# Kernel optimization log

Hardware: AMD Instinct MI355X
Metric: run time of the kernel (lower is better)

The kernel has to match this reference:

```python
import jax, jax.numpy as jnp
import numpy as np

IN_Q, OUT_Q = 32, 32
GRID_H, GRID_W = 64, 64
FREQ_H, FREQ_W = GRID_H, GRID_W // 2 + 1
BATCH = 32
INIT_SCALE = 0.02


def setup_inputs() -> dict:
    key = jax.random.key(0)
    keys = jax.random.split(key, 9)
    inp = {"x": jax.random.normal(keys[0], (BATCH, 4 * IN_Q, GRID_H, GRID_W), dtype=jnp.float32)}
    names = ["kr_w", "kr_x", "kr_y", "kr_z", "ki_w", "ki_x", "ki_y", "ki_z"]
    for i, n in enumerate(names):
        inp[n] = jax.random.normal(keys[i + 1], (IN_Q, OUT_Q, FREQ_H, FREQ_W), dtype=jnp.float32) * INIT_SCALE
    return inp


def reference(x, kr_w, kr_x, kr_y, kr_z, ki_w, ki_x, ki_y, ki_z):
    q = IN_Q
    # Split quaternion components and FFT each: [B, q, H, Wf] complex
    xs = jnp.stack([x[:, :q], x[:, q:2 * q], x[:, 2 * q:3 * q], x[:, 3 * q:]])  # [4,B,q,H,W]
    Xs = jnp.fft.rfft2(xs, s=(GRID_H, GRID_W), axes=(-2, -1))  # [4,B,q,H,Wf]
    # Complex kernels, stacked: [4, in_q, out_q, H, Wf]
    Ws = jnp.stack([kr_w + 1j * ki_w, kr_x + 1j * ki_x, kr_y + 1j * ki_y, kr_z + 1j * ki_z])
    # All 16 pairwise contractions in one einsum: C[p,q] = W_p contracted with X_q
    C = jnp.einsum('piohw,qbihw->pqbohw', Ws, Xs)  # [4,4,B,out,H,Wf]
    # Hamilton product combination
    Pw = C[0, 0] - C[1, 1] - C[2, 2] - C[3, 3]
    Px = C[0, 1] + C[1, 0] + C[2, 3] - C[3, 2]
    Py = C[0, 2] - C[1, 3] + C[2, 0] + C[3, 1]
    Pz = C[0, 3] + C[1, 2] - C[2, 1] + C[3, 0]
    P = jnp.stack([Pw, Px, Py, Pz])  # [4,B,out,H,Wf]
    o = jnp.fft.irfft2(P, s=(GRID_H, GRID_W), axes=(-2, -1))  # [4,B,out,H,W]
    # cat along channel dim: [B, 4*out, H, W]
    return jnp.concatenate([o[0], o[1], o[2], o[3]], axis=1)
```

## Files before the change

kernel.cpp:

```cpp
#include <hip/hip_runtime.h>

#define FH 64
#define FW 64
#define NWF 33
#define NBIN (FH*NWF)
#define NIMG 4096
#define PI2 6.283185307179586f

typedef unsigned short u16;
typedef unsigned int u32;
typedef __attribute__((ext_vector_type(8))) short bf16x8;
typedef __attribute__((ext_vector_type(8))) _Float16 f16x8;
typedef __attribute__((ext_vector_type(4))) unsigned short u16x4;
typedef __attribute__((ext_vector_type(4))) float f32x4;
typedef __attribute__((ext_vector_type(4))) int   i32x4;

__device__ __forceinline__ u16 f2bf(float f) {
    unsigned u = __float_as_uint(f);
    unsigned r = (u + 0x7FFFu + ((u >> 16) & 1u)) >> 16;
    return (u16)r;
}
__device__ __forceinline__ u16 f2h(float f) {
    _Float16 h = (_Float16)f;
    return __builtin_bit_cast(u16, h);
}
__device__ __forceinline__ float2 upk(u32 v) {
    return make_float2(__uint_as_float(v << 16), __uint_as_float(v & 0xFFFF0000u));
}
__device__ __forceinline__ u32 pk(float2 v) {
    return (u32)f2bf(v.x) | ((u32)f2bf(v.y) << 16);
}
__device__ __forceinline__ f16x8 negh(f16x8 v) {
    i32x4 t = __builtin_bit_cast(i32x4, v);
    t ^= (int)0x80008000;
    return __builtin_bit_cast(f16x8, t);
}

__global__ __launch_bounds__(512, 4) void fwd_prep_kernel(
    const float* __restrict__ x, u32* __restrict__ Xs,
    const float* __restrict__ s0, const float* __restrict__ s1,
    const float* __restrict__ s2, const float* __restrict__ s3,
    const float* __restrict__ s4, const float* __restrict__ s5,
    const float* __restrict__ s6, const float* __restrict__ s7,
    u16* __restrict__ WT)
{
    __shared__ __align__(16) u16 sm[36864];
    const int tid = threadIdx.x;

    if (blockIdx.x < 1024) {
        const int lane = tid & 63;
        const int wid  = tid >> 6;
        const int slot = wid >> 1;
        const int half = wid & 1;
        const int a16  = lane & 15;
        const int q    = lane >> 4;

        const int img = blockIdx.x * 4 + slot;
        const int qc = img >> 10;
        const int b  = (img >> 5) & 31;
        const int ci = img & 31;
        const float* __restrict__ src = x + ((size_t)b*128 + (size_t)qc*32 + ci) * (FH*FW);

        u16* mats0 = sm;
        u16* mats1 = sm + 64*72;
        u16* ST    = sm + 9216 + slot*6912;

        for (int t = tid; t < 4096; t += 512) {
            int a = t >> 6, bb = t & 63;
            float sn, cs;
            __sincosf(PI2 * (float)((a*bb) & 63) * (1.f/64.f), &sn, &cs);
            mats0[a*72 + bb] = f2h(cs);
            mats1[a*72 + bb] = f2h(sn);
        }

        f16x8 xf[2][2];
        #pragma unroll
        for (int mtl = 0; mtl < 2; ++mtl)
            #pragma unroll
            for (int ks = 0; ks < 2; ++ks) {
                const float* rp = src + (16*(2*half + mtl) + a16)*64 + ks*32 + q*8;
                float4 v0 = *(const float4*)rp;
                float4 v1 = *(const float4*)(rp + 4);
                xf[mtl][ks] = (f16x8){ (_Float16)v0.x, (_Float16)v0.y, (_Float16)v0.z, (_Float16)v0.w,
                                       (_Float16)v1.x, (_Float16)v1.y, (_Float16)v1.z, (_Float16)v1.w };
            }
        __syncthreads();

        #pragma unroll
        for (int mtl = 0; mtl < 2; ++mtl) {
            const int mt = 2*half + mtl;
            f32x4 are[3], aim[3];
            #pragma unroll
            for (int nt = 0; nt < 3; ++nt) { are[nt] = (f32x4){0,0,0,0}; aim[nt] = (f32x4){0,0,0,0}; }
            #pragma unroll
            for (int nt = 0; nt < 3; ++nt)
                #pragma unroll
                for (int ks = 0; ks < 2; ++ks) {
                    const int rb = (16*nt + a16)*72 + ks*32 + q*8;
                    f16x8 cf = *(const f16x8*)&mats0[rb];
                    f16x8 sf = *(const f16x8*)&mats1[rb];
                    are[nt] = __builtin_amdgcn_mfma_f32_16x16x32_f16(xf[mtl][ks], cf, are[nt], 0, 0, 0);
                    aim[nt] = __builtin_amdgcn_mfma_f32_16x16x32_f16(xf[mtl][ks], negh(sf), aim[nt], 0, 0, 0);
                }
            const int hb = 16*mt + 4*q;
            #pragma unroll
            for (int nt = 0; nt < 3; ++nt) {
                u16x4 re4 = { f2h(are[nt][0]), f2h(are[nt][1]), f2h(are[nt][2]), f2h(are[nt][3]) };
                u16x4 im4 = { f2h(aim[nt][0]), f2h(aim[nt][1]), f2h(aim[nt][2]), f2h(aim[nt][3]) };
                *(u16x4*)&ST[(16*nt + a16)*72 + hb]      = re4;
                *(u16x4*)&ST[(48 + 16*nt + a16)*72 + hb] = im4;
            }
        }
        __syncthreads();

        f16x8 bfr[2][3][2];
        #pragma unroll
        for (int ri = 0; ri < 2; ++ri)
            #pragma unroll
            for (int nt = 0; nt < 3; ++nt)
                #pragma unroll
                for (int ks = 0; ks < 2; ++ks)
                    bfr[ri][nt][ks] = *(const f16x8*)&ST[(ri*48 + 16*nt + a16)*72 + ks*32 + q*8];

        u32* __restrict__ dst = Xs + (size_t)img * NBIN;
        #pragma unroll
        for (int mtl = 0; mtl < 2; ++mtl) {
            const int mt = 2*half + mtl;
            f16x8 cfa[2], sfa[2], nsf[2];
            #pragma unroll
            for (int ks = 0; ks < 2; ++ks) {
                const int rb = (16*mt + a16)*72 + ks*32 + q*8;
                cfa[ks] = *(const f16x8*)&mats0[rb];
                sfa[ks] = *(const f16x8*)&mats1[rb];
                nsf[ks] = negh(sfa[ks]);
            }
            #pragma unroll
            for (int nt = 0; nt < 3; ++nt) {
                f32x4 xre = (f32x4){0,0,0,0}, xim = (f32x4){0,0,0,0};
                #pragma unroll
                for (int ks = 0; ks < 2; ++ks) {
                    xre = __builtin_amdgcn_mfma_f32_16x16x32_f16(cfa[ks], bfr[0][nt][ks], xre, 0, 0, 0);
                    xre = __builtin_amdgcn_mfma_f32_16x16x32_f16(sfa[ks], bfr[1][nt][ks], xre, 0, 0, 0);
                    xim = __builtin_amdgcn_mfma_f32_16x16x32_f16(cfa[ks], bfr[1][nt][ks], xim, 0, 0, 0);
                    xim = __builtin_amdgcn_mfma_f32_16x16x32_f16(nsf[ks], bfr[0][nt][ks], xim, 0, 0, 0);
                }
                const int k = 16*nt + a16;
                if (k < 33) {
                    #pragma unroll
                    for (int r = 0; r < 4; ++r)
                        dst[(16*mt + 4*q + r)*33 + k] = pk(make_float2(xre[r], xim[r]));
                }
            }
        }
    } else {
        const int pb = blockIdx.x - 1024;
        const int bt = pb % 66;
        const int ay = pb / 66;
        const int a  = ay >> 2;
        const int o0 = (ay & 3) * 8;
        const float* __restrict__ src =
            (a==0)?s0:(a==1)?s1:(a==2)?s2:(a==3)?s3:(a==4)?s4:(a==5)?s5:(a==6)?s6:s7;
        const int bin0 = bt * 32;
        u16* lds2 = sm;

        #pragma unroll
        for (int it = 0; it < 4; ++it) {
            int e = tid + it*512;
            int f4 = e & 7, rt = e >> 3;
            int i = rt & 31, oo = rt >> 5;
            int io = i*32 + o0 + oo;
            float4 v = ((const float4*)src)[(size_t)io*(NBIN/4) + bt*8 + f4];
            int chL = oo*32 + i;
            int bb = f4*4;
            lds2[(bb+0)*264 + chL] = f2bf(v.x);
            lds2[(bb+1)*264 + chL] = f2bf(v.y);
            lds2[(bb+2)*264 + chL] = f2bf(v.z);
            lds2[(bb+3)*264 + chL] = f2bf(v.w);
        }
        __syncthreads();
        const int p = a & 3, ri = a >> 2;
        #pragma unroll
        for (int it = 0; it < 2; ++it) {
            int e = tid + it*512;
            int binL = e >> 5, c8 = e & 31;
            bf16x8 v = *(const bf16x8*)&lds2[binL*264 + c8*8];
            size_t d = ((size_t)(bin0 + binL)*8 + p*2 + ri)*1024 + o0*32 + c8*8;
            *(bf16x8*)(WT + d) = v;
        }
    }
}

__global__ __launch_bounds__(256) void xpose_x_kernel(const u32* __restrict__ Xs,
                                                      u32* __restrict__ XT)
{
    const int g    = blockIdx.x;
    const int bin0 = blockIdx.y * 32;
    __shared__ u32 tile[32][33];
    const int tid = threadIdx.x;
    #pragma unroll
    for (int it = 0; it < 4; ++it) {
        int e = tid + it*256;
        int imgL = e >> 5, binL = e & 31;
        tile[imgL][binL] = Xs[(size_t)(g*32 + imgL) * NBIN + bin0 + binL];
    }
    __syncthreads();
    const int q = g >> 5, b = g & 31;
    #pragma unroll
    for (int it = 0; it < 2; ++it) {
        int e = tid + it*256;
        int binL = e >> 4, pr = e & 15;
        u32 v0 = tile[pr*2][binL], v1 = tile[pr*2 + 1][binL];
        u32 re = (v0 & 0xFFFFu) | (v1 << 16);
        u32 im = (v0 >> 16) | (v1 & 0xFFFF0000u);
        size_t base = ((size_t)(bin0 + binL)*8 + q*2) * 512 + b*16 + pr;
        XT[base]       = re;
        XT[base + 512] = im;
    }
}

__global__ __launch_bounds__(256) void contract_kernel(
    const u16* __restrict__ XT, const u16* __restrict__ WT,
    u32* __restrict__ P)
{
    const int bid  = blockIdx.x;
    const int bin  = (bid & 7) * (NBIN/8) + (bid >> 3);
    const int wid  = threadIdx.x >> 6;
    const int lane = threadIdx.x & 63;
    const int bh = wid >> 1, oh = wid & 1;
    const int row = lane & 15, kg = lane >> 4;

    const u16* __restrict__ xb = XT + (size_t)bin * 8192;
    const u16* __restrict__ wb = WT + (size_t)bin * 8192;

    bf16x8 ax[4][2];
    #pragma unroll
    for (int q = 0; q < 4; ++q)
        #pragma unroll
        for (int ri = 0; ri < 2; ++ri)
            ax[q][ri] = *(const bf16x8*)(xb + ((q*2 + ri)*32 + bh*16 + row)*32 + kg*8);

    bf16x8 wpos[4][2], wneg[4][2];
    #pragma unroll
    for (int p = 0; p < 4; ++p)
        #pragma unroll
        for (int ri = 0; ri < 2; ++ri) {
            bf16x8 w = *(const bf16x8*)(wb + ((p*2 + ri)*32 + oh*16 + row)*32 + kg*8);
            wpos[p][ri] = w;
            i32x4 t = __builtin_bit_cast(i32x4, w);
            t ^= (int)0x80008000;
            wneg[p][ri] = __builtin_bit_cast(bf16x8, t);
        }

    f32x4 acc[4][2];
    #pragma unroll
    for (int c = 0; c < 4; ++c)
        #pragma unroll
        for (int ri = 0; ri < 2; ++ri)
            acc[c][ri] = (f32x4){0.f, 0.f, 0.f, 0.f};

    constexpr int PI_[4][4] = {{0,1,2,3},{1,0,3,2},{2,3,0,1},{3,2,1,0}};
    constexpr int SG_[4][4] = {{1,-1,-1,-1},{1,1,-1,1},{1,1,1,-1},{1,-1,1,1}};
    #pragma unroll
    for (int c = 0; c < 4; ++c)
        #pragma unroll
        for (int q = 0; q < 4; ++q) {
            const int  p   = PI_[c][q];
            const bool pos = SG_[c][q] > 0;
            bf16x8 wr_s = pos ? wpos[p][0] : wneg[p][0];
            bf16x8 wi_s = pos ? wpos[p][1] : wneg[p][1];
            bf16x8 wi_m = pos ? wneg[p][1] : wpos[p][1];
            acc[c][0] = __builtin_amdgcn_mfma_f32_16x16x32_bf16(ax[q][0], wr_s, acc[c][0], 0, 0, 0);
            acc[c][0] = __builtin_amdgcn_mfma_f32_16x16x32_bf16(ax[q][1], wi_m, acc[c][0], 0, 0, 0);
            acc[c][1] = __builtin_amdgcn_mfma_f32_16x16x32_bf16(ax[q][1], wr_s, acc[c][1], 0, 0, 0);
            acc[c][1] = __builtin_amdgcn_mfma_f32_16x16x32_bf16(ax[q][0], wi_s, acc[c][1], 0, 0, 0);
        }

    u32* __restrict__ dst = P + (size_t)bin * 4096;
    #pragma unroll
    for (int c = 0; c < 4; ++c)
        #pragma unroll
        for (int r = 0; r < 4; ++r) {
            int b_ = bh*16 + kg*4 + r;
            int o  = oh*16 + row;
            dst[c*1024 + b_*32 + o] = pk(make_float2(acc[c][0][r], acc[c][1][r]));
        }
}

__global__ __launch_bounds__(512, 4) void fft_inv_kernel(const u32* __restrict__ P,
                                                         float* __restrict__ out)
{
    __shared__ __align__(16) u16 mats[2][64*72];
    __shared__ __align__(16) u16 wbuf[4][7168];

    const int tid  = threadIdx.x;
    const int lane = tid & 63;
    const int wid  = tid >> 6;
    const int slot = wid >> 1;
    const int half = wid & 1;
    const int ltid = (half << 6) | lane;
    const int a16  = lane & 15;
    const int q    = lane >> 4;

    const int bid = blockIdx.x;
    const int g   = (bid & 7) * 128 + (bid >> 3);
    const int img = g * 4 + slot;
    const int c  = img >> 10;
    const int b  = (img >> 5) & 31;
    const int oc = img & 31;

    for (int t = tid; t < 4096; t += 512) {
        int a = t >> 6, bb = t & 63;
        float sn, cs;
        __sincosf(PI2 * (float)((a*bb) & 63) * (1.f/64.f), &sn, &cs);
        mats[0][a*72 + bb] = f2h(cs);
        mats[1][a*72 + bb] = f2h(sn);
    }

    {
        u16* ETre = wbuf[slot];
        u16* ETim = wbuf[slot] + 48*72;
        for (int j = 33*72 + ltid; j < 48*72; j += 128) {
            ETre[j] = 0;
            ETim[j] = 0;
        }
    }
    for (int e = tid; e < NBIN*4; e += 512) {
        int bin = e >> 2, sl = e & 3;
        u32 v = P[(size_t)bin * 4096 + g*4 + sl];
        float2 f = upk(v);
        int hf = bin / 33, k = bin - hf*33;
        u16* ETre = wbuf[sl];
        u16* ETim = wbuf[sl] + 48*72;
        ETre[k*72 + hf] = f2h(f.x);
        ETim[k*72 + hf] = f2h(f.y);
    }
    __syncthreads();

    u16* ETre = wbuf[slot];
    u16* ETim = wbuf[slot] + 48*72;
    f16x8 ere[2][2], eim[2][2];
    #pragma unroll
    for (int mtl = 0; mtl < 2; ++mtl) {
        const int mt = 2*half + mtl;
        if (mt < 3) {
            #pragma unroll
            for (int ks = 0; ks < 2; ++ks) {
                ere[mtl][ks] = *(const f16x8*)&ETre[(16*mt + a16)*72 + ks*32 + q*8];
                eim[mtl][ks] = *(const f16x8*)&ETim[(16*mt + a16)*72 + ks*32 + q*8];
            }
        }
    }
    __syncthreads();

    u16* Tre = wbuf[slot];
    u16* Tim = wbuf[slot] + 64*56;
    #pragma unroll
    for (int mtl = 0; mtl < 2; ++mtl) {
        const int mt = 2*half + mtl;
        if (mt < 3) {
            #pragma unroll
            for (int nt = 0; nt < 4; ++nt) {
                f32x4 tre = (f32x4){0,0,0,0}, tim = (f32x4){0,0,0,0};
                #pragma unroll
                for (int ks = 0; ks < 2; ++ks) {
                    const int rb = (16*nt + a16)*72 + ks*32 + q*8;
                    f16x8 cf = *(const f16x8*)&mats[0][rb];
                    f16x8 sf = *(const f16x8*)&mats[1][rb];
                    tre = __builtin_amdgcn_mfma_f32_16x16x32_f16(ere[mtl][ks], cf, tre, 0, 0, 0);
                    tre = __builtin_amdgcn_mfma_f32_16x16x32_f16(eim[mtl][ks], negh(sf), tre, 0, 0, 0);
                    tim = __builtin_amdgcn_mfma_f32_16x16x32_f16(ere[mtl][ks], sf, tim, 0, 0, 0);
                    tim = __builtin_amdgcn_mfma_f32_16x16x32_f16(eim[mtl][ks], cf, tim, 0, 0, 0);
                }
                const int m0 = 16*mt + 4*q;
                u16x4 r4, i4;
                #pragma unroll
                for (int r = 0; r < 4; ++r) {
                    int m = m0 + r;
                    float s = (m == 0 || m == 32) ? (1.f/4096.f) : (2.f/4096.f);
                    r4[r] = (m < 33) ? f2h(tre[r] * s) : (u16)0;
                    i4[r] = (m < 33) ? f2h(tim[r] * s) : (u16)0;
                }
                *(u16x4*)&Tre[(16*nt + a16)*56 + m0] = r4;
                *(u16x4*)&Tim[(16*nt + a16)*56 + m0] = i4;
            }
        }
    }
    __syncthreads();

    float* __restrict__ dst = out + ((size_t)b*128 + (size_t)c*32 + oc) * (FH*FW);
    #pragma unroll
    for (int mtl = 0; mtl < 2; ++mtl) {
        const int mt = 2*half + mtl;
        f16x8 tfr[2], tfi[2];
        #pragma unroll
        for (int ks = 0; ks < 2; ++ks) {
            const int mbase = ks*32 + q*8;
            if (mbase < 48) {
                tfr[ks] = *(const f16x8*)&Tre[(16*mt + a16)*56 + mbase];
                tfi[ks] = *(const f16x8*)&Tim[(16*mt + a16)*56 + mbase];
            } else {
                tfr[ks] = (f16x8){0,0,0,0,0,0,0,0};
                tfi[ks] = (f16x8){0,0,0,0,0,0,0,0};
            }
        }
        #pragma unroll
        for (int nt = 0; nt < 4; ++nt) {
            f32x4 acc = (f32x4){0,0,0,0};
            #pragma unroll
            for (int ks = 0; ks < 2; ++ks) {
                const int rb = (16*nt + a16)*72 + ks*32 + q*8;
                f16x8 cf = *(const f16x8*)&mats[0][rb];
                f16x8 sf = *(const f16x8*)&mats[1][rb];
                acc = __builtin_amdgcn_mfma_f32_16x16x32_f16(tfr[ks], cf, acc, 0, 0, 0);
                acc = __builtin_amdgcn_mfma_f32_16x16x32_f16(tfi[ks], negh(sf), acc, 0, 0, 0);
            }
            #pragma unroll
            for (int r = 0; r < 4; ++r)
                dst[(16*mt + 4*q + r)*64 + 16*nt + a16] = acc[r];
        }
    }
}

extern "C" void kernel_launch(void* const* d_in, const int* in_sizes, int n_in,
                              void* d_out, int out_size, void* d_ws, size_t ws_size,
                              hipStream_t stream)
{
    const float* x   = (const float*)d_in[0];
    const float* krw = (const float*)d_in[1];
    const float* krx = (const float*)d_in[2];
    const float* kry = (const float*)d_in[3];
    const float* krz = (const float*)d_in[4];
    const float* kiw = (const float*)d_in[5];
    const float* kix = (const float*)d_in[6];
    const float* kiy = (const float*)d_in[7];
    const float* kiz = (const float*)d_in[8];

    const size_t R = (size_t)NBIN * 8192 * sizeof(u16);
    u16* XT = (u16*)d_ws;
    u16* WT = (u16*)((char*)d_ws + R);
    u32* Xs = (u32*)((char*)d_ws + 2*R);
    u32* P  = Xs;
    float* out = (float*)d_out;

    fwd_prep_kernel<<<dim3(1024 + 2112), 512, 0, stream>>>(x, Xs,
                                                           krw, krx, kry, krz,
                                                           kiw, kix, kiy, kiz, WT);
    xpose_x_kernel<<<dim3(128, NBIN/32), 256, 0, stream>>>(Xs, (u32*)XT);
    contract_kernel<<<dim3(NBIN), 256, 0, stream>>>(XT, WT, P);
    fft_inv_kernel<<<dim3(NIMG/4), 512, 0, stream>>>(P, out);
}
```

Measured before the change: 102.8 us.

## Process two image batches per FFT block and interleave FFT with weight-prep blocks

Each forward-FFT block now handles eight images in two rounds instead of four. It builds the twiddle table once for both rounds and issues the global loads for the second batch while the first batch's row pass is still running. Block indices are regrouped so that every 41 blocks hold 8 FFT blocks and 33 weight-transpose blocks, mixing compute-heavy and memory-heavy work across CUs. This adds barriers and register pressure and halves the number of FFT blocks.

```diff
diff --git a/kernel.cpp b/kernel.cpp
--- a/kernel.cpp
+++ b/kernel.cpp
@@ -46,8 +46,11 @@
 {
     __shared__ __align__(16) u16 sm[36864];
     const int tid = threadIdx.x;
-
-    if (blockIdx.x < 1024) {
+    const int grp = blockIdx.x / 41;
+    const int rem = blockIdx.x - grp*41;
+
+    if (rem < 8) {
+        const int fb = grp*8 + rem;
         const int lane = tid & 63;
         const int wid  = tid >> 6;
         const int slot = wid >> 1;
@@ -55,15 +58,14 @@
         const int a16  = lane & 15;
         const int q    = lane >> 4;
 
-        const int img = blockIdx.x * 4 + slot;
-        const int qc = img >> 10;
-        const int b  = (img >> 5) & 31;
-        const int ci = img & 31;
-        const float* __restrict__ src = x + ((size_t)b*128 + (size_t)qc*32 + ci) * (FH*FW);
-
         u16* mats0 = sm;
         u16* mats1 = sm + 64*72;
         u16* ST    = sm + 9216 + slot*6912;
+
+        const int imgA = fb*8 + slot;
+        const int imgB = fb*8 + 4 + slot;
+        const float* __restrict__ srcA = x + ((size_t)((imgA>>5)&31)*128 + (size_t)(imgA>>10)*32 + (imgA&31)) * (FH*FW);
+        const float* __restrict__ srcB = x + ((size_t)((imgB>>5)&31)*128 + (size_t)(imgB>>10)*32 + (imgB&31)) * (FH*FW);
 
         for (int t = tid; t < 4096; t += 512) {
             int a = t >> 6, bb = t & 63;
@@ -73,16 +75,16 @@
             mats1[a*72 + bb] = f2h(sn);
         }
 
-        f16x8 xf[2][2];
+        f16x8 xfA[2][2];
         #pragma unroll
         for (int mtl = 0; mtl < 2; ++mtl)
             #pragma unroll
             for (int ks = 0; ks < 2; ++ks) {
-                const float* rp = src + (16*(2*half + mtl) + a16)*64 + ks*32 + q*8;
+                const float* rp = srcA + (16*(2*half + mtl) + a16)*64 + ks*32 + q*8;
                 float4 v0 = *(const float4*)rp;
                 float4 v1 = *(const float4*)(rp + 4);
-                xf[mtl][ks] = (f16x8){ (_Float16)v0.x, (_Float16)v0.y, (_Float16)v0.z, (_Float16)v0.w,
-                                       (_Float16)v1.x, (_Float16)v1.y, (_Float16)v1.z, (_Float16)v1.w };
+                xfA[mtl][ks] = (f16x8){ (_Float16)v0.x, (_Float16)v0.y, (_Float16)v0.z, (_Float16)v0.w,
+                                        (_Float16)v1.x, (_Float16)v1.y, (_Float16)v1.z, (_Float16)v1.w };
             }
         __syncthreads();
 
@@ -99,8 +101,8 @@
                     const int rb = (16*nt + a16)*72 + ks*32 + q*8;
                     f16x8 cf = *(const f16x8*)&mats0[rb];
                     f16x8 sf = *(const f16x8*)&mats1[rb];
-                    are[nt] = __builtin_amdgcn_mfma_f32_16x16x32_f16(xf[mtl][ks], cf, are[nt], 0, 0, 0);
-                    aim[nt] = __builtin_amdgcn_mfma_f32_16x16x32_f16(xf[mtl][ks], negh(sf), aim[nt], 0, 0, 0);
+                    are[nt] = __builtin_amdgcn_mfma_f32_16x16x32_f16(xfA[mtl][ks], cf, are[nt], 0, 0, 0);
+                    aim[nt] = __builtin_amdgcn_mfma_f32_16x16x32_f16(xfA[mtl][ks], negh(sf), aim[nt], 0, 0, 0);
                 }
             const int hb = 16*mt + 4*q;
             #pragma unroll
@@ -111,6 +113,18 @@
                 *(u16x4*)&ST[(48 + 16*nt + a16)*72 + hb] = im4;
             }
         }
+
+        f16x8 xfB[2][2];
+        #pragma unroll
+        for (int mtl = 0; mtl < 2; ++mtl)
+            #pragma unroll
+            for (int ks = 0; ks < 2; ++ks) {
+                const float* rp = srcB + (16*(2*half + mtl) + a16)*64 + ks*32 + q*8;
+                float4 v0 = *(const float4*)rp;
+                float4 v1 = *(const float4*)(rp + 4);
+                xfB[mtl][ks] = (f16x8){ (_Float16)v0.x, (_Float16)v0.y, (_Float16)v0.z, (_Float16)v0.w,
+                                        (_Float16)v1.x, (_Float16)v1.y, (_Float16)v1.z, (_Float16)v1.w };
+            }
         __syncthreads();
 
         f16x8 bfr[2][3][2];
@@ -121,39 +135,110 @@
                 #pragma unroll
                 for (int ks = 0; ks < 2; ++ks)
                     bfr[ri][nt][ks] = *(const f16x8*)&ST[(ri*48 + 16*nt + a16)*72 + ks*32 + q*8];
-
-        u32* __restrict__ dst = Xs + (size_t)img * NBIN;
+        __syncthreads();
+
+        {
+            u32* __restrict__ dst = Xs + (size_t)imgA * NBIN;
+            #pragma unroll
+            for (int mtl = 0; mtl < 2; ++mtl) {
+                const int mt = 2*half + mtl;
+                f16x8 cfa[2], sfa[2], nsf[2];
+                #pragma unroll
+                for (int ks = 0; ks < 2; ++ks) {
+                    const int rb = (16*mt + a16)*72 + ks*32 + q*8;
+                    cfa[ks] = *(const f16x8*)&mats0[rb];
+                    sfa[ks] = *(const f16x8*)&mats1[rb];
+                    nsf[ks] = negh(sfa[ks]);
+                }
+                #pragma unroll
+                for (int nt = 0; nt < 3; ++nt) {
+                    f32x4 xre = (f32x4){0,0,0,0}, xim = (f32x4){0,0,0,0};
+                    #pragma unroll
+                    for (int ks = 0; ks < 2; ++ks) {
+                        xre = __builtin_amdgcn_mfma_f32_16x16x32_f16(cfa[ks], bfr[0][nt][ks], xre, 0, 0, 0);
+                        xre = __builtin_amdgcn_mfma_f32_16x16x32_f16(sfa[ks], bfr[1][nt][ks], xre, 0, 0, 0);
+                        xim = __builtin_amdgcn_mfma_f32_16x16x32_f16(cfa[ks], bfr[1][nt][ks], xim, 0, 0, 0);
+                        xim = __builtin_amdgcn_mfma_f32_16x16x32_f16(nsf[ks], bfr[0][nt][ks], xim, 0, 0, 0);
+                    }
+                    const int k = 16*nt + a16;
+                    if (k < 33) {
+                        #pragma unroll
+                        for (int r = 0; r < 4; ++r)
+                            dst[(16*mt + 4*q + r)*33 + k] = pk(make_float2(xre[r], xim[r]));
+                    }
+                }
+            }
+        }
+
         #pragma unroll
         for (int mtl = 0; mtl < 2; ++mtl) {
             const int mt = 2*half + mtl;
-            f16x8 cfa[2], sfa[2], nsf[2];
-            #pragma unroll
-            for (int ks = 0; ks < 2; ++ks) {
-                const int rb = (16*mt + a16)*72 + ks*32 + q*8;
-                cfa[ks] = *(const f16x8*)&mats0[rb];
-                sfa[ks] = *(const f16x8*)&mats1[rb];
-                nsf[ks] = negh(sfa[ks]);
-            }
+            f32x4 are[3], aim[3];
+            #pragma unroll
+            for (int nt = 0; nt < 3; ++nt) { are[nt] = (f32x4){0,0,0,0}; aim[nt] = (f32x4){0,0,0,0}; }
+            #pragma unroll
+            for (int nt = 0; nt < 3; ++nt)
+                #pragma unroll
+                for (int ks = 0; ks < 2; ++ks) {
+                    const int rb = (16*nt + a16)*72 + ks*32 + q*8;
+                    f16x8 cf = *(const f16x8*)&mats0[rb];
+                    f16x8 sf = *(const f16x8*)&mats1[rb];
+                    are[nt] = __builtin_amdgcn_mfma_f32_16x16x32_f16(xfB[mtl][ks], cf, are[nt], 0, 0, 0);
+                    aim[nt] = __builtin_amdgcn_mfma_f32_16x16x32_f16(xfB[mtl][ks], negh(sf), aim[nt], 0, 0, 0);
+                }
+            const int hb = 16*mt + 4*q;
             #pragma unroll
             for (int nt = 0; nt < 3; ++nt) {
-                f32x4 xre = (f32x4){0,0,0,0}, xim = (f32x4){0,0,0,0};
+                u16x4 re4 = { f2h(are[nt][0]), f2h(are[nt][1]), f2h(are[nt][2]), f2h(are[nt][3]) };
+                u16x4 im4 = { f2h(aim[nt][0]), f2h(aim[nt][1]), f2h(aim[nt][2]), f2h(aim[nt][3]) };
+                *(u16x4*)&ST[(16*nt + a16)*72 + hb]      = re4;
+                *(u16x4*)&ST[(48 + 16*nt + a16)*72 + hb] = im4;
+            }
+        }
+        __syncthreads();
+
+        #pragma unroll
+        for (int ri = 0; ri < 2; ++ri)
+            #pragma unroll
+            for (int nt = 0; nt < 3; ++nt)
+                #pragma unroll
+                for (int ks = 0; ks < 2; ++ks)
+                    bfr[ri][nt][ks] = *(const f16x8*)&ST[(ri*48 + 16*nt + a16)*72 + ks*32 + q*8];
+
+        {
+            u32* __restrict__ dst = Xs + (size_t)imgB * NBIN;
+            #pragma unroll
+            for (int mtl = 0; mtl < 2; ++mtl) {
+                const int mt = 2*half + mtl;
+                f16x8 cfa[2], sfa[2], nsf[2];
                 #pragma unroll
                 for (int ks = 0; ks < 2; ++ks) {
-                    xre = __builtin_amdgcn_mfma_f32_16x16x32_f16(cfa[ks], bfr[0][nt][ks], xre, 0, 0, 0);
-                    xre = __builtin_amdgcn_mfma_f32_16x16x32_f16(sfa[ks], bfr[1][nt][ks], xre, 0, 0, 0);
-                    xim = __builtin_amdgcn_mfma_f32_16x16x32_f16(cfa[ks], bfr[1][nt][ks], xim, 0, 0, 0);
-                    xim = __builtin_amdgcn_mfma_f32_16x16x32_f16(nsf[ks], bfr[0][nt][ks], xim, 0, 0, 0);
-                }
-                const int k = 16*nt + a16;
-                if (k < 33) {
+                    const int rb = (16*mt + a16)*72 + ks*32 + q*8;
+                    cfa[ks] = *(const f16x8*)&mats0[rb];
+                    sfa[ks] = *(const f16x8*)&mats1[rb];
+                    nsf[ks] = negh(sfa[ks]);
+                }
+                #pragma unroll
+                for (int nt = 0; nt < 3; ++nt) {
+                    f32x4 xre = (f32x4){0,0,0,0}, xim = (f32x4){0,0,0,0};
                     #pragma unroll
-                    for (int r = 0; r < 4; ++r)
-                        dst[(16*mt + 4*q + r)*33 + k] = pk(make_float2(xre[r], xim[r]));
+                    for (int ks = 0; ks < 2; ++ks) {
+                        xre = __builtin_amdgcn_mfma_f32_16x16x32_f16(cfa[ks], bfr[0][nt][ks], xre, 0, 0, 0);
+                        xre = __builtin_amdgcn_mfma_f32_16x16x32_f16(sfa[ks], bfr[1][nt][ks], xre, 0, 0, 0);
+                        xim = __builtin_amdgcn_mfma_f32_16x16x32_f16(cfa[ks], bfr[1][nt][ks], xim, 0, 0, 0);
+                        xim = __builtin_amdgcn_mfma_f32_16x16x32_f16(nsf[ks], bfr[0][nt][ks], xim, 0, 0, 0);
+                    }
+                    const int k = 16*nt + a16;
+                    if (k < 33) {
+                        #pragma unroll
+                        for (int r = 0; r < 4; ++r)
+                            dst[(16*mt + 4*q + r)*33 + k] = pk(make_float2(xre[r], xim[r]));
+                    }
                 }
             }
         }
     } else {
-        const int pb = blockIdx.x - 1024;
+        const int pb = grp*33 + (rem - 8);
         const int bt = pb % 66;
         const int ay = pb / 66;
         const int a  = ay >> 2;
@@ -442,9 +527,9 @@
     u32* P  = Xs;
     float* out = (float*)d_out;
 
-    fwd_prep_kernel<<<dim3(1024 + 2112), 512, 0, stream>>>(x, Xs,
-                                                           krw, krx, kry, krz,
-                                                           kiw, kix, kiy, kiz, WT);
+    fwd_prep_kernel<<<dim3(2624), 512, 0, stream>>>(x, Xs,
+                                                    krw, krx, kry, krz,
+                                                    kiw, kix, kiy, kiz, WT);
     xpose_x_kernel<<<dim3(128, NBIN/32), 256, 0, stream>>>(Xs, (u32*)XT);
     contract_kernel<<<dim3(NBIN), 256, 0, stream>>>(XT, WT, P);
     fft_inv_kernel<<<dim3(NIMG/4), 512, 0, stream>>>(P, out);
```

Result: slower. 111.9 us (+8.9%).
